# Optimization experiments

Hardware: AMD Instinct MI355X
Metric: run time of the kernel (lower is better)

## Reference

```python
import jax, jax.numpy as jnp
import numpy as np

F = 20000; S = 60000; U = 2000; I = 2000
NSUP = S + U + I
DEG = 8; E = NSUP * DEG
HID = 128; NH = 8; DH = HID // NH
SE = 256; UE = 128; IE = 128
FFN = 512; NITER = 1
SV = 100000; UV = 5000; IV = 5000


def _gat_ffn(h_src, h_dst, src, dst, ew, n_dst, W, al, ar, ae, W1, b1, W2, b2, g, b):
    # multi-head GAT with scalar edge-weight term + position-wise FFN (pre-LN residual)
    z_src = jnp.einsum('nd,hde->nhe', h_src, W)   # [Nsrc, NH, DH]
    z_dst = jnp.einsum('nd,hde->nhe', h_dst, W)   # [Ndst, NH, DH]
    el = jnp.einsum('nhe,he->nh', z_src, al)
    er = jnp.einsum('nhe,he->nh', z_dst, ar)
    e = jax.nn.leaky_relu(el[src] + er[dst] + ew[:, None] * ae[None, :], 0.2)  # [E, NH]
    m = jax.ops.segment_max(e, dst, num_segments=n_dst)
    m = jnp.where(jnp.isfinite(m), m, 0.0)
    ex = jnp.exp(e - m[dst])
    den = jax.ops.segment_sum(ex, dst, num_segments=n_dst)
    alpha = ex / jnp.maximum(den[dst], 1e-9)                       # edge softmax per dst
    out = jax.ops.segment_sum(alpha[:, :, None] * z_src[src], dst, num_segments=n_dst)
    h = jax.nn.elu(out.reshape(n_dst, NH * DH))
    mu = h.mean(-1, keepdims=True)
    v = ((h - mu) ** 2).mean(-1, keepdims=True)
    ln = (h - mu) * jax.lax.rsqrt(v + 1e-6) * g + b
    return h + (jnp.maximum(ln @ W1 + b1, 0.0) @ W2 + b2)


def setup_inputs() -> dict:
    key = jax.random.key(0)
    ks = jax.random.split(key, 40)
    d = {}
    d['fid'] = jax.random.randint(ks[0], (F,), 0, F)
    d['sid'] = jax.random.randint(ks[1], (S,), 0, SV)
    d['uid'] = jax.random.randint(ks[2], (U,), 0, UV)
    d['iid'] = jax.random.randint(ks[3], (I,), 0, IV)
    d['e_src'] = jax.random.randint(ks[4], (E,), 0, F)
    d['e_dst'] = jnp.repeat(jnp.arange(NSUP), DEG)   # fixed in-degree, every supernode covered
    d['e_w'] = jax.random.uniform(ks[5], (E,), jnp.float32)
    def n(i, shape, s=0.05):
        return jax.random.normal(ks[i], shape, jnp.float32) * s
    d['feat_tab'] = n(6, (F, HID), 1.0)
    d['sent_tab'] = n(7, (SV, SE), 1.0)
    d['user_tab'] = n(8, (UV, UE), 1.0)
    d['item_tab'] = n(9, (IV, IE), 1.0)
    d['Wsp'] = n(10, (SE, HID)); d['bsp'] = n(11, (HID,))
    d['Wup'] = n(12, (UE, HID)); d['Wip'] = n(13, (IE, HID))
    names = ['W', 'al', 'ar', 'ae', 'W1', 'b1', 'W2', 'b2', 'g', 'b']
    shapes = [(NH, HID, DH), (NH, DH), (NH, DH), (NH,), (HID, FFN), (FFN,), (FFN, HID), (HID,), (HID,), (HID,)]
    k = 14
    for pre in ['w2s_', 's2w_']:
        for nm, sh in zip(names, shapes):
            d[pre + nm] = n(k, sh); k += 1
    d['w2s_g'] = jnp.ones((HID,)); d['s2w_g'] = jnp.ones((HID,))
    d['whW'] = n(34, (HID, 2)); d['whb'] = n(35, (2,))
    return d


def reference(fid, sid, uid, iid, e_src, e_dst, e_w, feat_tab, sent_tab, user_tab, item_tab,
              Wsp, bsp, Wup, Wip,
              w2s_W, w2s_al, w2s_ar, w2s_ae, w2s_W1, w2s_b1, w2s_W2, w2s_b2, w2s_g, w2s_b,
              s2w_W, s2w_al, s2w_ar, s2w_ae, s2w_W1, s2w_b1, s2w_W2, s2w_b2, s2w_g, s2w_b,
              whW, whb):
    feat_init = feat_tab[fid]                     # feature init_state == its embedding
    sent_init = sent_tab[sid] @ Wsp + bsp         # sent_state_proj
    # mean of predecessor feature init_states per supernode (set_unembed / set_inembed)
    fsum = jax.ops.segment_sum(feat_init[e_src], e_dst, num_segments=NSUP)
    cnt = jax.ops.segment_sum(jnp.ones((E,), feat_init.dtype), e_dst, num_segments=NSUP)
    fmean = fsum / jnp.maximum(cnt, 1.0)[:, None]
    user_init = (user_tab[uid] + fmean[S:S + U]) @ Wup
    item_init = (item_tab[iid] + fmean[S + U:]) @ Wip
    sup = jnp.concatenate([sent_init, user_init, item_init], axis=0)  # [NSUP, HID]
    feat = feat_init
    p_w2s = (w2s_W, w2s_al, w2s_ar, w2s_ae, w2s_W1, w2s_b1, w2s_W2, w2s_b2, w2s_g, w2s_b)
    p_s2w = (s2w_W, s2w_al, s2w_ar, s2w_ae, s2w_W1, s2w_b1, s2w_W2, s2w_b2, s2w_g, s2w_b)
    sup = _gat_ffn(feat, sup, e_src, e_dst, e_w, NSUP, *p_w2s)        # feature2sent
    for _ in range(NITER):
        feat = _gat_ffn(sup, feat, e_dst, e_src, e_w, F, *p_s2w)      # sent2feature (reversed edges)
        sup = _gat_ffn(feat, sup, e_src, e_dst, e_w, NSUP, *p_w2s)    # feature2sent
    return sup[:S] @ whW + whb                    # wh on sentence nodes -> [S, 2]
```

## Files before the change

kernel.cpp:

```cpp
#include <hip/hip_runtime.h>
#include <hip/hip_bf16.h>

constexpr int F_N   = 20000;
constexpr int S_N   = 60000;
constexpr int U_N   = 2000;
constexpr int I_N   = 2000;
constexpr int NSUPN = 64000;
constexpr int E_NN  = NSUPN * 8;

typedef __bf16 bf16_t;
typedef bf16_t bf16x8 __attribute__((ext_vector_type(8)));
typedef float  f32x4  __attribute__((ext_vector_type(4)));


__global__ void k_gather128(const float* __restrict__ tab, const int* __restrict__ idx,
                            float* __restrict__ out, int M) {
  int t = blockIdx.x * 256 + threadIdx.x;
  if (t >= M * 128) return;
  int r = t >> 7, c = t & 127;
  out[t] = tab[(size_t)idx[r] * 128 + c];
}

__global__ void k_fmean(const float* __restrict__ feat, const int* __restrict__ esrc,
                        float* __restrict__ fm) {
  int n = S_N + blockIdx.x;
  int c = threadIdx.x;
  float s = 0.f;
#pragma unroll
  for (int j = 0; j < 8; ++j) s += feat[(size_t)esrc[n * 8 + j] * 128 + c];
  fm[(size_t)blockIdx.x * 128 + c] = s * 0.125f;
}

__global__ void k_addgather(const float* __restrict__ tab, const int* __restrict__ idx,
                            const float* __restrict__ fm, int fmoff,
                            float* __restrict__ out, int M) {
  int t = blockIdx.x * 256 + threadIdx.x;
  if (t >= M * 128) return;
  int r = t >> 7, c = t & 127;
  out[t] = tab[(size_t)idx[r] * 128 + c] + fm[(size_t)(fmoff + r) * 128 + c];
}

__global__ void k_conv_t_split(const float* __restrict__ in, bf16_t* __restrict__ hi,
                               bf16_t* __restrict__ lo, int K, int C) {
  int t = blockIdx.x * 256 + threadIdx.x;
  if (t >= K * C) return;
  int c = t / K, k = t - c * K;
  float v = in[(size_t)k * C + c];
  bf16_t h = (bf16_t)v;
  hi[t] = h;
  lo[t] = (bf16_t)(v - (float)h);
}

__global__ void k_build_wft_split(const float* __restrict__ W, bf16_t* __restrict__ hi,
                                  bf16_t* __restrict__ lo) {
  int t = blockIdx.x * 256 + threadIdx.x;
  if (t >= 128 * 128) return;
  int col = t >> 7, d = t & 127;
  float v = W[((col >> 4) << 11) + (d << 4) + (col & 15)];
  bf16_t h = (bf16_t)v;
  hi[t] = h;
  lo[t] = (bf16_t)(v - (float)h);
}

template<bool GATHER, bool BIAS>
__global__ __launch_bounds__(128)
void k_gemm_rows(const float* __restrict__ A, const int* __restrict__ gidx, int ldA,
                 const float* __restrict__ B, const float* __restrict__ bias,
                 float* __restrict__ C, int K) {
  __shared__ float As[16 * 256];
  int r0 = blockIdx.x * 16;
  int tid = threadIdx.x;
  for (int idx = tid; idx < 16 * K; idx += 128) {
    int r = idx / K, k = idx - r * K;
    int row = r0 + r;
    size_t abase = GATHER ? (size_t)gidx[row] * ldA : (size_t)row * ldA;
    As[r * K + k] = A[abase + k];
  }
  __syncthreads();
  float acc[16];
#pragma unroll
  for (int r = 0; r < 16; ++r) acc[r] = 0.f;
  int c = tid;
  for (int k = 0; k < K; ++k) {
    float w = B[k * 128 + c];
#pragma unroll
    for (int r = 0; r < 16; ++r) acc[r] += As[r * K + k] * w;
  }
  float bv = BIAS ? bias[c] : 0.f;
#pragma unroll
  for (int r = 0; r < 16; ++r) C[(size_t)(r0 + r) * 128 + c] = acc[r] + bv;
}

__global__ __launch_bounds__(256)
void k_sent_mfma(const float* __restrict__ tab, const int* __restrict__ sid,
                 const bf16_t* __restrict__ Bhi, const bf16_t* __restrict__ Blo,
                 const float* __restrict__ bias, float* __restrict__ out) {
  __shared__ bf16_t Ahi[32][256];
  __shared__ bf16_t Alo[32][256];
  int r0 = blockIdx.x * 32;
  int tid = threadIdx.x;
  for (int i = 0; i < 4; ++i) {
    int cid = tid + 256 * i;
    int r = cid >> 5, c0 = (cid & 31) * 8;
    const float* src = &tab[(size_t)sid[r0 + r] * 256 + c0];
    float4 v0 = *(const float4*)src, v1 = *(const float4*)(src + 4);
    float vv[8] = {v0.x, v0.y, v0.z, v0.w, v1.x, v1.y, v1.z, v1.w};
    bf16x8 hv, lv;
#pragma unroll
    for (int j = 0; j < 8; ++j) {
      bf16_t hb = (bf16_t)vv[j];
      hv[j] = hb;
      lv[j] = (bf16_t)(vv[j] - (float)hb);
    }
    int cs = c0 ^ ((r & 7) << 3);
    *(bf16x8*)&Ahi[r][cs] = hv;
    *(bf16x8*)&Alo[r][cs] = lv;
  }
  __syncthreads();
  int w = tid >> 6, l = tid & 63, la = l & 15, lb = l >> 4;
  int swz = (la & 7) << 3;
  f32x4 acc[2][2] = {};
#pragma unroll
  for (int ks = 0; ks < 8; ++ks) {
    int k0 = ks * 32 + lb * 8;
    int ka = k0 ^ swz;
    bf16x8 ah0 = *(const bf16x8*)&Ahi[la][ka];
    bf16x8 ah1 = *(const bf16x8*)&Ahi[16 + la][ka];
    bf16x8 al0 = *(const bf16x8*)&Alo[la][ka];
    bf16x8 al1 = *(const bf16x8*)&Alo[16 + la][ka];
#pragma unroll
    for (int ct = 0; ct < 2; ++ct) {
      int col = w * 32 + ct * 16 + la;
      bf16x8 bh = *(const bf16x8*)&Bhi[(size_t)col * 256 + k0];
      bf16x8 bl = *(const bf16x8*)&Blo[(size_t)col * 256 + k0];
      acc[0][ct] = __builtin_amdgcn_mfma_f32_16x16x32_bf16(ah0, bh, acc[0][ct], 0, 0, 0);
      acc[0][ct] = __builtin_amdgcn_mfma_f32_16x16x32_bf16(ah0, bl, acc[0][ct], 0, 0, 0);
      acc[0][ct] = __builtin_amdgcn_mfma_f32_16x16x32_bf16(al0, bh, acc[0][ct], 0, 0, 0);
      acc[1][ct] = __builtin_amdgcn_mfma_f32_16x16x32_bf16(ah1, bh, acc[1][ct], 0, 0, 0);
      acc[1][ct] = __builtin_amdgcn_mfma_f32_16x16x32_bf16(ah1, bl, acc[1][ct], 0, 0, 0);
      acc[1][ct] = __builtin_amdgcn_mfma_f32_16x16x32_bf16(al1, bh, acc[1][ct], 0, 0, 0);
    }
  }
#pragma unroll
  for (int ct = 0; ct < 2; ++ct) {
    int col = w * 32 + ct * 16 + la;
    float bv = bias[col];
#pragma unroll
    for (int rt = 0; rt < 2; ++rt)
#pragma unroll
      for (int r = 0; r < 4; ++r)
        out[(size_t)(r0 + rt * 16 + lb * 4 + r) * 128 + col] = acc[rt][ct][r] + bv;
  }
}

__global__ __launch_bounds__(256)
void k_zproj_mfma(const float* __restrict__ h, const bf16_t* __restrict__ WftH,
                  const bf16_t* __restrict__ WftL, float* __restrict__ z) {
  __shared__ bf16_t hbH[32][128];
  __shared__ bf16_t hbL[32][128];
  int r0 = blockIdx.x * 32;
  int tid = threadIdx.x;
  for (int i = 0; i < 2; ++i) {
    int cid = tid + 256 * i;
    int r = cid >> 4, c0 = (cid & 15) * 8;
    const float* src = &h[(size_t)(r0 + r) * 128 + c0];
    float4 v0 = *(const float4*)src;
    float4 v1 = *(const float4*)(src + 4);
    float vv[8] = {v0.x, v0.y, v0.z, v0.w, v1.x, v1.y, v1.z, v1.w};
    bf16x8 hv, lv;
#pragma unroll
    for (int j = 0; j < 8; ++j) {
      bf16_t hb = (bf16_t)vv[j];
      hv[j] = hb;
      lv[j] = (bf16_t)(vv[j] - (float)hb);
    }
    int cs = c0 ^ ((r & 7) << 3);
    *(bf16x8*)&hbH[r][cs] = hv;
    *(bf16x8*)&hbL[r][cs] = lv;
  }
  __syncthreads();
  int w = tid >> 6, l = tid & 63, la = l & 15, lb = l >> 4;
  int swz = (la & 7) << 3;
  f32x4 acc[2][2] = {};
#pragma unroll
  for (int ks = 0; ks < 4; ++ks) {
    int k0 = ks * 32 + lb * 8;
    int ka = k0 ^ swz;
    bf16x8 ah0 = *(const bf16x8*)&hbH[la][ka];
    bf16x8 ah1 = *(const bf16x8*)&hbH[16 + la][ka];
    bf16x8 al0 = *(const bf16x8*)&hbL[la][ka];
    bf16x8 al1 = *(const bf16x8*)&hbL[16 + la][ka];
#pragma unroll
    for (int ct = 0; ct < 2; ++ct) {
      int col = w * 32 + ct * 16 + la;
      bf16x8 bh = *(const bf16x8*)&WftH[(size_t)col * 128 + k0];
      bf16x8 bl = *(const bf16x8*)&WftL[(size_t)col * 128 + k0];
      acc[0][ct] = __builtin_amdgcn_mfma_f32_16x16x32_bf16(ah0, bh, acc[0][ct], 0, 0, 0);
      acc[0][ct] = __builtin_amdgcn_mfma_f32_16x16x32_bf16(ah0, bl, acc[0][ct], 0, 0, 0);
      acc[0][ct] = __builtin_amdgcn_mfma_f32_16x16x32_bf16(al0, bh, acc[0][ct], 0, 0, 0);
      acc[1][ct] = __builtin_amdgcn_mfma_f32_16x16x32_bf16(ah1, bh, acc[1][ct], 0, 0, 0);
      acc[1][ct] = __builtin_amdgcn_mfma_f32_16x16x32_bf16(ah1, bl, acc[1][ct], 0, 0, 0);
      acc[1][ct] = __builtin_amdgcn_mfma_f32_16x16x32_bf16(al1, bh, acc[1][ct], 0, 0, 0);
    }
  }
#pragma unroll
  for (int ct = 0; ct < 2; ++ct) {
    int col = w * 32 + ct * 16 + la;
#pragma unroll
    for (int rt = 0; rt < 2; ++rt)
#pragma unroll
      for (int r = 0; r < 4; ++r)
        z[(size_t)(r0 + rt * 16 + lb * 4 + r) * 128 + col] = acc[rt][ct][r];
  }
}

__global__ void k_el(const float* __restrict__ z, const float* __restrict__ a,
                     float* __restrict__ el, int N) {
  int t = blockIdx.x * 256 + threadIdx.x;
  if (t >= N * 8) return;
  int r = t >> 3, h = t & 7;
  const float* zr = z + (size_t)r * 128 + h * 16;
  const float* ah = a + h * 16;
  float s = 0.f;
#pragma unroll
  for (int e = 0; e < 16; ++e) s += zr[e] * ah[e];
  el[t] = s;
}

__global__ void k_logits_w2s(const float* __restrict__ el, const float* __restrict__ er,
                             const int* __restrict__ esrc, const float* __restrict__ ew,
                             const float* __restrict__ ae, float* __restrict__ lg) {
  int t = blockIdx.x * 256 + threadIdx.x;
  if (t >= E_NN * 8) return;
  int eid = t >> 3, h = t & 7;
  float x = el[(size_t)esrc[eid] * 8 + h] + er[(size_t)(eid >> 3) * 8 + h] + ew[eid] * ae[h];
  lg[t] = x > 0.f ? x : 0.2f * x;
}
__global__ void k_logits_s2w(const float* __restrict__ el, const float* __restrict__ er,
                             const int* __restrict__ eids, const int* __restrict__ pdst,
                             const float* __restrict__ ew, const float* __restrict__ ae,
                             float* __restrict__ lg) {
  int t = blockIdx.x * 256 + threadIdx.x;
  if (t >= E_NN * 8) return;
  int q = t >> 3, h = t & 7;
  int eid = eids[q];
  float x = el[(size_t)(eid >> 3) * 8 + h] + er[(size_t)pdst[q] * 8 + h] + ew[eid] * ae[h];
  lg[t] = x > 0.f ? x : 0.2f * x;
}

__global__ __launch_bounds__(256)
void k_attn8_v2(const float* __restrict__ zsrc, const float* __restrict__ lg,
                const int* __restrict__ esrc, float* __restrict__ hout) {
  int half = threadIdx.x >> 7;
  int n = blockIdx.x * 2 + half;
  int c = threadIdx.x & 127;
  int h = c >> 4;
  int s[8];
#pragma unroll
  for (int j = 0; j < 8; ++j) s[j] = esrc[n * 8 + j];
  float lv[8];
#pragma unroll
  for (int j = 0; j < 8; ++j) lv[j] = lg[(size_t)n * 64 + j * 8 + h];
  float m = -1e30f;
#pragma unroll
  for (int j = 0; j < 8; ++j) m = fmaxf(m, lv[j]);
  float den = 0.f;
#pragma unroll
  for (int j = 0; j < 8; ++j) { lv[j] = __expf(lv[j] - m); den += lv[j]; }
  float inv = 1.f / fmaxf(den, 1e-9f);
  float acc = 0.f;
#pragma unroll
  for (int j = 0; j < 8; ++j) acc += lv[j] * zsrc[(size_t)s[j] * 128 + c];
  acc *= inv;
  hout[(size_t)n * 128 + c] = acc > 0.f ? acc : (__expf(acc) - 1.f);
}

__global__ __launch_bounds__(128)
void k_attn_csr2(const float* __restrict__ zsrc, const float* __restrict__ lg,
                 const int* __restrict__ rowptr, const int* __restrict__ eids,
                 float* __restrict__ hout) {
  constexpr int CHUNK = 128;
  __shared__ float alg[CHUNK][8];
  __shared__ int   svs[CHUNK];
  int n = blockIdx.x;
  int c = threadIdx.x;
  int h = c >> 4;
  int beg = rowptr[n], deg = rowptr[n + 1] - beg;
  float acc = 0.f, mh = -1e30f, denh = 0.f;
  for (int c0 = 0; c0 < deg; c0 += CHUNK) {
    int cn = min(CHUNK, deg - c0);
    __syncthreads();
    for (int idx = c; idx < cn * 8; idx += 128)
      alg[idx >> 3][idx & 7] = lg[(size_t)(beg + c0) * 8 + idx];
    for (int j = c; j < cn; j += 128)
      svs[j] = eids[beg + c0 + j] >> 3;
    __syncthreads();
    float cm = mh;
    for (int j = 0; j < cn; ++j) cm = fmaxf(cm, alg[j][h]);
    float scale = __expf(mh - cm);
    acc *= scale; denh *= scale; mh = cm;
#pragma unroll 4
    for (int j = 0; j < cn; ++j) {
      float p = __expf(alg[j][h] - mh);
      denh += p;
      acc += p * zsrc[(size_t)svs[j] * 128 + c];
    }
  }
  acc /= fmaxf(denh, 1e-9f);
  hout[(size_t)n * 128 + c] = acc > 0.f ? acc : (__expf(acc) - 1.f);
}

__global__ __launch_bounds__(256)
void k_ln_ffn_mfma(const float* __restrict__ h, const float* __restrict__ g,
                   const float* __restrict__ b,
                   const bf16_t* __restrict__ W1tH, const bf16_t* __restrict__ W1tL,
                   const float* __restrict__ b1,
                   const bf16_t* __restrict__ W2tH, const bf16_t* __restrict__ W2tL,
                   const float* __restrict__ b2,
                   float* __restrict__ out) {
  __shared__ float  hs[32][128];
  __shared__ bf16_t lnbH[32][128];
  __shared__ bf16_t lnbL[32][128];
  __shared__ bf16_t mid[32][512];
  int r0 = blockIdx.x * 32;
  int tid = threadIdx.x;
  for (int i = 0; i < 4; ++i) {
    int cid = tid + 256 * i;
    int r = cid >> 5, c0 = (cid & 31) * 4;
    *(float4*)&hs[r][c0] = *(const float4*)&h[(size_t)(r0 + r) * 128 + c0];
  }
  __syncthreads();
  {
    int r = tid >> 3, lane = tid & 7;
    float sum = 0.f, sq = 0.f;
    for (int c = lane; c < 128; c += 8) { float v = hs[r][c]; sum += v; sq += v * v; }
#pragma unroll
    for (int o = 4; o >= 1; o >>= 1) { sum += __shfl_xor(sum, o); sq += __shfl_xor(sq, o); }
    float mu = sum * (1.f / 128.f);
    float var = sq * (1.f / 128.f) - mu * mu;
    float inv = rsqrtf(var + 1e-6f);
    int sw = (r & 7) << 3;
    for (int c = lane; c < 128; c += 8) {
      float v = (hs[r][c] - mu) * inv * g[c] + b[c];
      bf16_t hh = (bf16_t)v;
      lnbH[r][c ^ sw] = hh;
      lnbL[r][c ^ sw] = (bf16_t)(v - (float)hh);
    }
  }
  __syncthreads();
  int w = tid >> 6, l = tid & 63, la = l & 15, lb = l >> 4;
  int swz = (la & 7) << 3;
  {
    f32x4 acc1[2][8] = {};
#pragma unroll
    for (int ks = 0; ks < 4; ++ks) {
      int k0 = ks * 32 + lb * 8;
      int ka = k0 ^ swz;
      bf16x8 ah0 = *(const bf16x8*)&lnbH[la][ka];
      bf16x8 ah1 = *(const bf16x8*)&lnbH[16 + la][ka];
      bf16x8 al0 = *(const bf16x8*)&lnbL[la][ka];
      bf16x8 al1 = *(const bf16x8*)&lnbL[16 + la][ka];
#pragma unroll
      for (int ct = 0; ct < 8; ++ct) {
        int col = w * 128 + ct * 16 + la;
        bf16x8 bh = *(const bf16x8*)&W1tH[(size_t)col * 128 + k0];
        bf16x8 bl = *(const bf16x8*)&W1tL[(size_t)col * 128 + k0];
        acc1[0][ct] = __builtin_amdgcn_mfma_f32_16x16x32_bf16(ah0, bh, acc1[0][ct], 0, 0, 0);
        acc1[0][ct] = __builtin_amdgcn_mfma_f32_16x16x32_bf16(ah0, bl, acc1[0][ct], 0, 0, 0);
        acc1[0][ct] = __builtin_amdgcn_mfma_f32_16x16x32_bf16(al0, bh, acc1[0][ct], 0, 0, 0);
        acc1[1][ct] = __builtin_amdgcn_mfma_f32_16x16x32_bf16(ah1, bh, acc1[1][ct], 0, 0, 0);
        acc1[1][ct] = __builtin_amdgcn_mfma_f32_16x16x32_bf16(ah1, bl, acc1[1][ct], 0, 0, 0);
        acc1[1][ct] = __builtin_amdgcn_mfma_f32_16x16x32_bf16(al1, bh, acc1[1][ct], 0, 0, 0);
      }
    }
#pragma unroll
    for (int ct = 0; ct < 8; ++ct) {
      int col = w * 128 + ct * 16 + la;
      float bv = b1[col];
#pragma unroll
      for (int rt = 0; rt < 2; ++rt)
#pragma unroll
        for (int r = 0; r < 4; ++r) {
          int row = rt * 16 + lb * 4 + r;
          float v = acc1[rt][ct][r] + bv;
          mid[row][col ^ ((row & 7) << 3)] = (bf16_t)fmaxf(v, 0.f);
        }
    }
  }
  __syncthreads();
  {
    f32x4 acc2[2][2] = {};
#pragma unroll
    for (int ks = 0; ks < 16; ++ks) {
      int k0 = ks * 32 + lb * 8;
      int ka = k0 ^ swz;
      bf16x8 a0 = *(const bf16x8*)&mid[la][ka];
      bf16x8 a1 = *(const bf16x8*)&mid[16 + la][ka];
#pragma unroll
      for (int ct = 0; ct < 2; ++ct) {
        int col = w * 32 + ct * 16 + la;
        bf16x8 bh = *(const bf16x8*)&W2tH[(size_t)col * 512 + k0];
        bf16x8 bl = *(const bf16x8*)&W2tL[(size_t)col * 512 + k0];
        acc2[0][ct] = __builtin_amdgcn_mfma_f32_16x16x32_bf16(a0, bh, acc2[0][ct], 0, 0, 0);
        acc2[0][ct] = __builtin_amdgcn_mfma_f32_16x16x32_bf16(a0, bl, acc2[0][ct], 0, 0, 0);
        acc2[1][ct] = __builtin_amdgcn_mfma_f32_16x16x32_bf16(a1, bh, acc2[1][ct], 0, 0, 0);
        acc2[1][ct] = __builtin_amdgcn_mfma_f32_16x16x32_bf16(a1, bl, acc2[1][ct], 0, 0, 0);
      }
    }
#pragma unroll
    for (int ct = 0; ct < 2; ++ct) {
      int col = w * 32 + ct * 16 + la;
      float bv = b2[col];
#pragma unroll
      for (int rt = 0; rt < 2; ++rt)
#pragma unroll
        for (int r = 0; r < 4; ++r) {
          int row = rt * 16 + lb * 4 + r;
          out[(size_t)(r0 + row) * 128 + col] = hs[row][col] + acc2[rt][ct][r] + bv;
        }
    }
  }
}

__global__ __launch_bounds__(256)
void k_whout(const float* __restrict__ sup, const float* __restrict__ whW,
             const float* __restrict__ whb, float* __restrict__ out) {
  int wv = threadIdx.x >> 6, lane = threadIdx.x & 63;
  int r = blockIdx.x * 4 + wv;
  if (r >= S_N) return;
  const float* row = sup + (size_t)r * 128;
  float a0 = 0.f, a1 = 0.f;
  for (int d = lane; d < 128; d += 64) {
    float v = row[d];
    a0 += v * whW[d * 2];
    a1 += v * whW[d * 2 + 1];
  }
#pragma unroll
  for (int o = 32; o >= 1; o >>= 1) { a0 += __shfl_xor(a0, o); a1 += __shfl_xor(a1, o); }
  if (lane == 0) { out[r * 2] = a0 + whb[0]; out[r * 2 + 1] = a1 + whb[1]; }
}

__global__ void k_count(const int* __restrict__ esrc, int* __restrict__ counts) {
  int t = blockIdx.x * 256 + threadIdx.x;
  if (t < E_NN) atomicAdd(&counts[esrc[t]], 1);
}

__global__ __launch_bounds__(1024)
void k_scan(const int* __restrict__ counts, int* __restrict__ rowptr) {
  __shared__ int wsum[16];
  __shared__ int carry;
  int tid = threadIdx.x, lane = tid & 63, w = tid >> 6;
  if (tid == 0) { carry = 0; rowptr[0] = 0; }
  __syncthreads();
  for (int base = 0; base < F_N; base += 1024) {
    int i = base + tid;
    int v = (i < F_N) ? counts[i] : 0;
    int s = v;
#pragma unroll
    for (int o = 1; o < 64; o <<= 1) { int t2 = __shfl_up(s, o); if (lane >= o) s += t2; }
    if (lane == 63) wsum[w] = s;
    __syncthreads();
    if (w == 0) {
      int t2 = (lane < 16) ? wsum[lane] : 0;
#pragma unroll
      for (int o = 1; o < 16; o <<= 1) { int u = __shfl_up(t2, o); if (lane >= o) t2 += u; }
      if (lane < 16) wsum[lane] = t2;
    }
    __syncthreads();
    int add = carry + (w > 0 ? wsum[w - 1] : 0);
    if (i < F_N) rowptr[i + 1] = s + add;
    int total = wsum[15];
    __syncthreads();
    if (tid == 0) carry += total;
    __syncthreads();
  }
}

__global__ void k_fill(const int* __restrict__ esrc, const int* __restrict__ rowptr,
                       int* __restrict__ fill, int* __restrict__ eids,
                       int* __restrict__ pdst) {
  int t = blockIdx.x * 256 + threadIdx.x;
  if (t < E_NN) {
    int sv = esrc[t];
    int p = atomicAdd(&fill[sv], 1);
    eids[rowptr[sv] + p] = t;
    pdst[rowptr[sv] + p] = sv;
  }
}

extern "C" void kernel_launch(void* const* d_in, const int* in_sizes, int n_in,
                              void* d_out, int out_size, void* d_ws, size_t ws_size,
                              hipStream_t stream) {
  const int* fid = (const int*)d_in[0];
  const int* sid = (const int*)d_in[1];
  const int* uid = (const int*)d_in[2];
  const int* iid = (const int*)d_in[3];
  const int* e_src = (const int*)d_in[4];
  const int* e_dst = (const int*)d_in[5];
  const float* e_w = (const float*)d_in[6];
  const float* feat_tab = (const float*)d_in[7];
  const float* sent_tab = (const float*)d_in[8];
  const float* user_tab = (const float*)d_in[9];
  const float* item_tab = (const float*)d_in[10];
  const float* Wsp = (const float*)d_in[11];
  const float* bsp = (const float*)d_in[12];
  const float* Wup = (const float*)d_in[13];
  const float* Wip = (const float*)d_in[14];
  const float* w2s[10]; for (int i = 0; i < 10; ++i) w2s[i] = (const float*)d_in[15 + i];
  const float* s2w[10]; for (int i = 0; i < 10; ++i) s2w[i] = (const float*)d_in[25 + i];
  const float* whW = (const float*)d_in[35];
  const float* whb = (const float*)d_in[36];
  float* out = (float*)d_out;

  char* wp = (char*)d_ws;
  auto alloc = [&](size_t nbytes) -> void* {
    void* p = (void*)wp;
    wp += (nbytes + 255) & ~(size_t)255;
    return p;
  };
  bf16_t* WftHA = (bf16_t*)alloc(128 * 128 * 2);
  bf16_t* WftLA = (bf16_t*)alloc(128 * 128 * 2);
  bf16_t* WftHB = (bf16_t*)alloc(128 * 128 * 2);
  bf16_t* WftLB = (bf16_t*)alloc(128 * 128 * 2);
  bf16_t* W1tHA = (bf16_t*)alloc(512 * 128 * 2);
  bf16_t* W1tLA = (bf16_t*)alloc(512 * 128 * 2);
  bf16_t* W1tHB = (bf16_t*)alloc(512 * 128 * 2);
  bf16_t* W1tLB = (bf16_t*)alloc(512 * 128 * 2);
  bf16_t* W2tHA = (bf16_t*)alloc(512 * 128 * 2);
  bf16_t* W2tLA = (bf16_t*)alloc(512 * 128 * 2);
  bf16_t* W2tHB = (bf16_t*)alloc(512 * 128 * 2);
  bf16_t* W2tLB = (bf16_t*)alloc(512 * 128 * 2);
  bf16_t* WspH  = (bf16_t*)alloc(128 * 256 * 2);
  bf16_t* WspL  = (bf16_t*)alloc(128 * 256 * 2);
  int* rowptr  = (int*)alloc((size_t)(F_N + 1) * 4);
  int* cnts    = (int*)alloc((size_t)2 * F_N * 4);
  int* eids    = (int*)alloc((size_t)E_NN * 4);
  int* pdst    = (int*)alloc((size_t)E_NN * 4);
  float* featA = (float*)alloc((size_t)F_N * 128 * 4);
  float* supA  = (float*)alloc((size_t)NSUPN * 128 * 4);
  float* zf    = (float*)alloc((size_t)F_N * 128 * 4);
  float* zs    = (float*)alloc((size_t)NSUPN * 128 * 4);
  float* hbuf  = (float*)alloc((size_t)NSUPN * 128 * 4);
  float* elbig = (float*)alloc((size_t)NSUPN * 8 * 4);
  float* erbig = (float*)alloc((size_t)NSUPN * 8 * 4);
  float* lgbuf = (float*)alloc((size_t)E_NN * 8 * 4);
  float* atmpu = (float*)alloc((size_t)U_N * 128 * 4);
  float* atmpi = (float*)alloc((size_t)I_N * 128 * 4);
  float* fm    = (float*)alloc((size_t)(U_N + I_N) * 128 * 4);

  k_build_wft_split<<<64, 256, 0, stream>>>(w2s[0], WftHA, WftLA);
  k_build_wft_split<<<64, 256, 0, stream>>>(s2w[0], WftHB, WftLB);
  k_conv_t_split<<<(512 * 128 + 255) / 256, 256, 0, stream>>>(w2s[4], W1tHA, W1tLA, 128, 512);
  k_conv_t_split<<<(512 * 128 + 255) / 256, 256, 0, stream>>>(s2w[4], W1tHB, W1tLB, 128, 512);
  k_conv_t_split<<<(512 * 128 + 255) / 256, 256, 0, stream>>>(w2s[6], W2tHA, W2tLA, 512, 128);
  k_conv_t_split<<<(512 * 128 + 255) / 256, 256, 0, stream>>>(s2w[6], W2tHB, W2tLB, 512, 128);
  k_conv_t_split<<<(256 * 128 + 255) / 256, 256, 0, stream>>>(Wsp, WspH, WspL, 256, 128);

  k_gather128<<<(F_N * 128 + 255) / 256, 256, 0, stream>>>(feat_tab, fid, featA, F_N);
  k_fmean<<<U_N + I_N, 128, 0, stream>>>(featA, e_src, fm);
  k_sent_mfma<<<S_N / 32, 256, 0, stream>>>(sent_tab, sid, WspH, WspL, bsp, supA);
  k_addgather<<<(U_N * 128 + 255) / 256, 256, 0, stream>>>(user_tab, uid, fm, 0, atmpu, U_N);
  k_gemm_rows<false, false><<<U_N / 16, 128, 0, stream>>>(atmpu, nullptr, 128, Wup, nullptr,
                                                          supA + (size_t)S_N * 128, 128);
  k_addgather<<<(I_N * 128 + 255) / 256, 256, 0, stream>>>(item_tab, iid, fm, U_N, atmpi, I_N);
  k_gemm_rows<false, false><<<I_N / 16, 128, 0, stream>>>(atmpi, nullptr, 128, Wip, nullptr,
                                                          supA + (size_t)(S_N + U_N) * 128, 128);
  hipMemsetAsync(cnts, 0, (size_t)2 * F_N * 4, stream);
  k_count<<<(E_NN + 255) / 256, 256, 0, stream>>>(e_src, cnts);
  k_scan<<<1, 1024, 0, stream>>>(cnts, rowptr);
  k_fill<<<(E_NN + 255) / 256, 256, 0, stream>>>(e_src, rowptr, cnts + F_N, eids, pdst);

  auto gat_w2s = [&](const float* hsrc, const float* hdst, float* outp) {
    k_zproj_mfma<<<F_N / 32, 256, 0, stream>>>(hsrc, WftHA, WftLA, zf);
    k_zproj_mfma<<<NSUPN / 32, 256, 0, stream>>>(hdst, WftHA, WftLA, zs);
    k_el<<<(F_N * 8 + 255) / 256, 256, 0, stream>>>(zf, w2s[1], elbig, F_N);
    k_el<<<(NSUPN * 8 + 255) / 256, 256, 0, stream>>>(zs, w2s[2], erbig, NSUPN);
    k_logits_w2s<<<(E_NN * 8 + 255) / 256, 256, 0, stream>>>(elbig, erbig, e_src, e_w, w2s[3], lgbuf);
    k_attn8_v2<<<NSUPN / 2, 256, 0, stream>>>(zf, lgbuf, e_src, hbuf);
    k_ln_ffn_mfma<<<NSUPN / 32, 256, 0, stream>>>(hbuf, w2s[8], w2s[9], W1tHA, W1tLA, w2s[5],
                                                  W2tHA, W2tLA, w2s[7], outp);
  };
  auto gat_s2w = [&](const float* hsrc, const float* hdst, float* outp) {
    k_zproj_mfma<<<NSUPN / 32, 256, 0, stream>>>(hsrc, WftHB, WftLB, zs);
    k_zproj_mfma<<<F_N / 32, 256, 0, stream>>>(hdst, WftHB, WftLB, zf);
    k_el<<<(NSUPN * 8 + 255) / 256, 256, 0, stream>>>(zs, s2w[1], elbig, NSUPN);
    k_el<<<(F_N * 8 + 255) / 256, 256, 0, stream>>>(zf, s2w[2], erbig, F_N);
    k_logits_s2w<<<(E_NN * 8 + 255) / 256, 256, 0, stream>>>(elbig, erbig, eids, pdst, e_w, s2w[3], lgbuf);
    k_attn_csr2<<<F_N, 128, 0, stream>>>(zs, lgbuf, rowptr, eids, hbuf);
    k_ln_ffn_mfma<<<F_N / 32, 256, 0, stream>>>(hbuf, s2w[8], s2w[9], W1tHB, W1tLB, s2w[5],
                                                W2tHB, W2tLB, s2w[7], outp);
  };

  gat_w2s(featA, supA, supA);
  gat_s2w(supA, featA, featA);
  gat_w2s(featA, supA, supA);

  k_whout<<<(S_N + 3) / 4, 256, 0, stream>>>(supA, whW, whb, out);
}
```

Before: 783.4 us.

## Skip non-sentence rows in final GAT, rework LN-FFN tile, sort CSR rows

New measurement: 1.064 ms. +35.9%, slower.

```diff
diff --git a/kernel.cpp b/kernel.cpp
--- a/kernel.cpp
+++ b/kernel.cpp
@@ -1,5 +1,6 @@
 #include <hip/hip_runtime.h>
 #include <hip/hip_bf16.h>
+#include <math.h>
 
 constexpr int F_N   = 20000;
 constexpr int S_N   = 60000;
@@ -229,9 +230,9 @@
 
 __global__ void k_logits_w2s(const float* __restrict__ el, const float* __restrict__ er,
                              const int* __restrict__ esrc, const float* __restrict__ ew,
-                             const float* __restrict__ ae, float* __restrict__ lg) {
-  int t = blockIdx.x * 256 + threadIdx.x;
-  if (t >= E_NN * 8) return;
+                             const float* __restrict__ ae, float* __restrict__ lg, int nE) {
+  int t = blockIdx.x * 256 + threadIdx.x;
+  if (t >= nE * 8) return;
   int eid = t >> 3, h = t & 7;
   float x = el[(size_t)esrc[eid] * 8 + h] + er[(size_t)(eid >> 3) * 8 + h] + ew[eid] * ae[h];
   lg[t] = x > 0.f ? x : 0.2f * x;
@@ -266,13 +267,13 @@
   for (int j = 0; j < 8; ++j) m = fmaxf(m, lv[j]);
   float den = 0.f;
 #pragma unroll
-  for (int j = 0; j < 8; ++j) { lv[j] = __expf(lv[j] - m); den += lv[j]; }
+  for (int j = 0; j < 8; ++j) { lv[j] = expf(lv[j] - m); den += lv[j]; }
   float inv = 1.f / fmaxf(den, 1e-9f);
   float acc = 0.f;
 #pragma unroll
   for (int j = 0; j < 8; ++j) acc += lv[j] * zsrc[(size_t)s[j] * 128 + c];
   acc *= inv;
-  hout[(size_t)n * 128 + c] = acc > 0.f ? acc : (__expf(acc) - 1.f);
+  hout[(size_t)n * 128 + c] = acc > 0.f ? acc : expm1f(acc);
 }
 
 __global__ __launch_bounds__(128)
@@ -297,80 +298,88 @@
     __syncthreads();
     float cm = mh;
     for (int j = 0; j < cn; ++j) cm = fmaxf(cm, alg[j][h]);
-    float scale = __expf(mh - cm);
+    float scale = expf(mh - cm);
     acc *= scale; denh *= scale; mh = cm;
 #pragma unroll 4
     for (int j = 0; j < cn; ++j) {
-      float p = __expf(alg[j][h] - mh);
+      float p = expf(alg[j][h] - mh);
       denh += p;
       acc += p * zsrc[(size_t)svs[j] * 128 + c];
     }
   }
   acc /= fmaxf(denh, 1e-9f);
-  hout[(size_t)n * 128 + c] = acc > 0.f ? acc : (__expf(acc) - 1.f);
-}
-
-__global__ __launch_bounds__(256)
-void k_ln_ffn_mfma(const float* __restrict__ h, const float* __restrict__ g,
-                   const float* __restrict__ b,
-                   const bf16_t* __restrict__ W1tH, const bf16_t* __restrict__ W1tL,
-                   const float* __restrict__ b1,
-                   const bf16_t* __restrict__ W2tH, const bf16_t* __restrict__ W2tL,
-                   const float* __restrict__ b2,
-                   float* __restrict__ out) {
-  __shared__ float  hs[32][128];
-  __shared__ bf16_t lnbH[32][128];
-  __shared__ bf16_t lnbL[32][128];
-  __shared__ bf16_t mid[32][512];
-  int r0 = blockIdx.x * 32;
+  hout[(size_t)n * 128 + c] = acc > 0.f ? acc : expm1f(acc);
+}
+
+__global__ __launch_bounds__(256, 4)
+void k_ln_ffn3(const float* __restrict__ h, const float* __restrict__ g,
+               const float* __restrict__ b,
+               const bf16_t* __restrict__ W1tH, const bf16_t* __restrict__ W1tL,
+               const float* __restrict__ b1,
+               const bf16_t* __restrict__ W2tH, const bf16_t* __restrict__ W2tL,
+               const float* __restrict__ b2,
+               float* __restrict__ out) {
+  __shared__ bf16_t lnbH[16][128];
+  __shared__ bf16_t lnbL[16][128];
+  __shared__ bf16_t midH[16][512];
+  __shared__ bf16_t midL[16][512];
+  int r0 = blockIdx.x * 16;
   int tid = threadIdx.x;
-  for (int i = 0; i < 4; ++i) {
-    int cid = tid + 256 * i;
-    int r = cid >> 5, c0 = (cid & 31) * 4;
-    *(float4*)&hs[r][c0] = *(const float4*)&h[(size_t)(r0 + r) * 128 + c0];
-  }
-  __syncthreads();
   {
-    int r = tid >> 3, lane = tid & 7;
-    float sum = 0.f, sq = 0.f;
-    for (int c = lane; c < 128; c += 8) { float v = hs[r][c]; sum += v; sq += v * v; }
-#pragma unroll
-    for (int o = 4; o >= 1; o >>= 1) { sum += __shfl_xor(sum, o); sq += __shfl_xor(sq, o); }
+    int r = tid >> 4, lane = tid & 15;
+    int c0 = lane * 8;
+    const float* hrow = &h[(size_t)(r0 + r) * 128 + c0];
+    float4 t0 = *(const float4*)hrow;
+    float4 t1 = *(const float4*)(hrow + 4);
+    float v[8] = {t0.x, t0.y, t0.z, t0.w, t1.x, t1.y, t1.z, t1.w};
+    float sum = 0.f;
+#pragma unroll
+    for (int j = 0; j < 8; ++j) sum += v[j];
+#pragma unroll
+    for (int o = 8; o >= 1; o >>= 1) sum += __shfl_xor(sum, o);
     float mu = sum * (1.f / 128.f);
-    float var = sq * (1.f / 128.f) - mu * mu;
-    float inv = rsqrtf(var + 1e-6f);
-    int sw = (r & 7) << 3;
-    for (int c = lane; c < 128; c += 8) {
-      float v = (hs[r][c] - mu) * inv * g[c] + b[c];
-      bf16_t hh = (bf16_t)v;
-      lnbH[r][c ^ sw] = hh;
-      lnbL[r][c ^ sw] = (bf16_t)(v - (float)hh);
-    }
+    float sq = 0.f;
+#pragma unroll
+    for (int j = 0; j < 8; ++j) { float d = v[j] - mu; sq += d * d; }
+#pragma unroll
+    for (int o = 8; o >= 1; o >>= 1) sq += __shfl_xor(sq, o);
+    float var = sq * (1.f / 128.f);
+    float inv = 1.f / sqrtf(var + 1e-6f);
+    float4 gv0 = *(const float4*)(g + c0), gv1 = *(const float4*)(g + c0 + 4);
+    float4 bv0 = *(const float4*)(b + c0), bv1 = *(const float4*)(b + c0 + 4);
+    float gg[8] = {gv0.x, gv0.y, gv0.z, gv0.w, gv1.x, gv1.y, gv1.z, gv1.w};
+    float bb[8] = {bv0.x, bv0.y, bv0.z, bv0.w, bv1.x, bv1.y, bv1.z, bv1.w};
+    bf16x8 ho, lo;
+#pragma unroll
+    for (int j = 0; j < 8; ++j) {
+      float lnv = (v[j] - mu) * inv * gg[j] + bb[j];
+      bf16_t hh = (bf16_t)lnv;
+      ho[j] = hh;
+      lo[j] = (bf16_t)(lnv - (float)hh);
+    }
+    int cs = c0 ^ ((r & 7) << 3);
+    *(bf16x8*)&lnbH[r][cs] = ho;
+    *(bf16x8*)&lnbL[r][cs] = lo;
   }
   __syncthreads();
   int w = tid >> 6, l = tid & 63, la = l & 15, lb = l >> 4;
   int swz = (la & 7) << 3;
   {
-    f32x4 acc1[2][8] = {};
+    f32x4 acc1[8] = {};
 #pragma unroll
     for (int ks = 0; ks < 4; ++ks) {
       int k0 = ks * 32 + lb * 8;
       int ka = k0 ^ swz;
-      bf16x8 ah0 = *(const bf16x8*)&lnbH[la][ka];
-      bf16x8 ah1 = *(const bf16x8*)&lnbH[16 + la][ka];
-      bf16x8 al0 = *(const bf16x8*)&lnbL[la][ka];
-      bf16x8 al1 = *(const bf16x8*)&lnbL[16 + la][ka];
+      bf16x8 ah = *(const bf16x8*)&lnbH[la][ka];
+      bf16x8 al = *(const bf16x8*)&lnbL[la][ka];
 #pragma unroll
       for (int ct = 0; ct < 8; ++ct) {
         int col = w * 128 + ct * 16 + la;
         bf16x8 bh = *(const bf16x8*)&W1tH[(size_t)col * 128 + k0];
         bf16x8 bl = *(const bf16x8*)&W1tL[(size_t)col * 128 + k0];
-        acc1[0][ct] = __builtin_amdgcn_mfma_f32_16x16x32_bf16(ah0, bh, acc1[0][ct], 0, 0, 0);
-        acc1[0][ct] = __builtin_amdgcn_mfma_f32_16x16x32_bf16(ah0, bl, acc1[0][ct], 0, 0, 0);
-        acc1[0][ct] = __builtin_amdgcn_mfma_f32_16x16x32_bf16(al0, bh, acc1[0][ct], 0, 0, 0);
-        acc1[1][ct] = __builtin_amdgcn_mfma_f32_16x16x32_bf16(ah1, bh, acc1[1][ct], 0, 0, 0);
-        acc1[1][ct] = __builtin_amdgcn_mfma_f32_16x16x32_bf16(ah1, bl, acc1[1][ct], 0, 0, 0);
-        acc1[1][ct] = __builtin_amdgcn_mfma_f32_16x16x32_bf16(al1, bh, acc1[1][ct], 0, 0, 0);
+        acc1[ct] = __builtin_amdgcn_mfma_f32_16x16x32_bf16(ah, bh, acc1[ct], 0, 0, 0);
+        acc1[ct] = __builtin_amdgcn_mfma_f32_16x16x32_bf16(ah, bl, acc1[ct], 0, 0, 0);
+        acc1[ct] = __builtin_amdgcn_mfma_f32_16x16x32_bf16(al, bh, acc1[ct], 0, 0, 0);
       }
     }
 #pragma unroll
@@ -378,46 +387,43 @@
       int col = w * 128 + ct * 16 + la;
       float bv = b1[col];
 #pragma unroll
-      for (int rt = 0; rt < 2; ++rt)
-#pragma unroll
-        for (int r = 0; r < 4; ++r) {
-          int row = rt * 16 + lb * 4 + r;
-          float v = acc1[rt][ct][r] + bv;
-          mid[row][col ^ ((row & 7) << 3)] = (bf16_t)fmaxf(v, 0.f);
-        }
+      for (int r = 0; r < 4; ++r) {
+        int row = lb * 4 + r;
+        float v = fmaxf(acc1[ct][r] + bv, 0.f);
+        bf16_t hh = (bf16_t)v;
+        int cs = col ^ ((row & 7) << 3);
+        midH[row][cs] = hh;
+        midL[row][cs] = (bf16_t)(v - (float)hh);
+      }
     }
   }
   __syncthreads();
-  {
-    f32x4 acc2[2][2] = {};
-#pragma unroll
-    for (int ks = 0; ks < 16; ++ks) {
-      int k0 = ks * 32 + lb * 8;
-      int ka = k0 ^ swz;
-      bf16x8 a0 = *(const bf16x8*)&mid[la][ka];
-      bf16x8 a1 = *(const bf16x8*)&mid[16 + la][ka];
-#pragma unroll
-      for (int ct = 0; ct < 2; ++ct) {
-        int col = w * 32 + ct * 16 + la;
-        bf16x8 bh = *(const bf16x8*)&W2tH[(size_t)col * 512 + k0];
-        bf16x8 bl = *(const bf16x8*)&W2tL[(size_t)col * 512 + k0];
-        acc2[0][ct] = __builtin_amdgcn_mfma_f32_16x16x32_bf16(a0, bh, acc2[0][ct], 0, 0, 0);
-        acc2[0][ct] = __builtin_amdgcn_mfma_f32_16x16x32_bf16(a0, bl, acc2[0][ct], 0, 0, 0);
-        acc2[1][ct] = __builtin_amdgcn_mfma_f32_16x16x32_bf16(a1, bh, acc2[1][ct], 0, 0, 0);
-        acc2[1][ct] = __builtin_amdgcn_mfma_f32_16x16x32_bf16(a1, bl, acc2[1][ct], 0, 0, 0);
-      }
-    }
+  f32x4 acc2[2] = {};
+#pragma unroll
+  for (int ks = 0; ks < 16; ++ks) {
+    int k0 = ks * 32 + lb * 8;
+    int ka = k0 ^ swz;
+    bf16x8 ah = *(const bf16x8*)&midH[la][ka];
+    bf16x8 al = *(const bf16x8*)&midL[la][ka];
 #pragma unroll
     for (int ct = 0; ct < 2; ++ct) {
       int col = w * 32 + ct * 16 + la;
-      float bv = b2[col];
-#pragma unroll
-      for (int rt = 0; rt < 2; ++rt)
-#pragma unroll
-        for (int r = 0; r < 4; ++r) {
-          int row = rt * 16 + lb * 4 + r;
-          out[(size_t)(r0 + row) * 128 + col] = hs[row][col] + acc2[rt][ct][r] + bv;
-        }
+      bf16x8 bh = *(const bf16x8*)&W2tH[(size_t)col * 512 + k0];
+      bf16x8 bl = *(const bf16x8*)&W2tL[(size_t)col * 512 + k0];
+      acc2[ct] = __builtin_amdgcn_mfma_f32_16x16x32_bf16(ah, bh, acc2[ct], 0, 0, 0);
+      acc2[ct] = __builtin_amdgcn_mfma_f32_16x16x32_bf16(ah, bl, acc2[ct], 0, 0, 0);
+      acc2[ct] = __builtin_amdgcn_mfma_f32_16x16x32_bf16(al, bh, acc2[ct], 0, 0, 0);
+    }
+  }
+#pragma unroll
+  for (int ct = 0; ct < 2; ++ct) {
+    int col = w * 32 + ct * 16 + la;
+    float bv = b2[col];
+#pragma unroll
+    for (int r = 0; r < 4; ++r) {
+      int row = lb * 4 + r;
+      size_t gi = (size_t)(r0 + row) * 128 + col;
+      out[gi] = h[gi] + acc2[ct][r] + bv;
     }
   }
 }
@@ -486,6 +492,32 @@
     eids[rowptr[sv] + p] = t;
     pdst[rowptr[sv] + p] = sv;
   }
+}
+
+__global__ __launch_bounds__(256)
+void k_sort_rows(const int* __restrict__ rowptr, int* __restrict__ eids) {
+  __shared__ int buf[1024];
+  int n = blockIdx.x;
+  int beg = rowptr[n], deg = rowptr[n + 1] - beg;
+  if (deg <= 1 || deg > 1024) return;
+  int m = 1; while (m < deg) m <<= 1;
+  for (int i = threadIdx.x; i < m; i += 256)
+    buf[i] = (i < deg) ? eids[beg + i] : 0x7fffffff;
+  __syncthreads();
+  for (int k = 2; k <= m; k <<= 1) {
+    for (int j = k >> 1; j > 0; j >>= 1) {
+      for (int i = threadIdx.x; i < m; i += 256) {
+        int ixj = i ^ j;
+        if (ixj > i) {
+          int a = buf[i], bv = buf[ixj];
+          bool up = ((i & k) == 0);
+          if ((a > bv) == up) { buf[i] = bv; buf[ixj] = a; }
+        }
+      }
+      __syncthreads();
+    }
+  }
+  for (int i = threadIdx.x; i < deg; i += 256) eids[beg + i] = buf[i];
 }
 
 extern "C" void kernel_launch(void* const* d_in, const int* in_sizes, int n_in,
@@ -569,16 +601,19 @@
   k_count<<<(E_NN + 255) / 256, 256, 0, stream>>>(e_src, cnts);
   k_scan<<<1, 1024, 0, stream>>>(cnts, rowptr);
   k_fill<<<(E_NN + 255) / 256, 256, 0, stream>>>(e_src, rowptr, cnts + F_N, eids, pdst);
-
-  auto gat_w2s = [&](const float* hsrc, const float* hdst, float* outp) {
+  k_sort_rows<<<F_N, 256, 0, stream>>>(rowptr, eids);
+
+  auto gat_w2s = [&](const float* hsrc, const float* hdst, float* outp, bool last) {
+    int ndst = last ? S_N : NSUPN;
     k_zproj_mfma<<<F_N / 32, 256, 0, stream>>>(hsrc, WftHA, WftLA, zf);
-    k_zproj_mfma<<<NSUPN / 32, 256, 0, stream>>>(hdst, WftHA, WftLA, zs);
+    k_zproj_mfma<<<ndst / 32, 256, 0, stream>>>(hdst, WftHA, WftLA, zs);
     k_el<<<(F_N * 8 + 255) / 256, 256, 0, stream>>>(zf, w2s[1], elbig, F_N);
-    k_el<<<(NSUPN * 8 + 255) / 256, 256, 0, stream>>>(zs, w2s[2], erbig, NSUPN);
-    k_logits_w2s<<<(E_NN * 8 + 255) / 256, 256, 0, stream>>>(elbig, erbig, e_src, e_w, w2s[3], lgbuf);
-    k_attn8_v2<<<NSUPN / 2, 256, 0, stream>>>(zf, lgbuf, e_src, hbuf);
-    k_ln_ffn_mfma<<<NSUPN / 32, 256, 0, stream>>>(hbuf, w2s[8], w2s[9], W1tHA, W1tLA, w2s[5],
-                                                  W2tHA, W2tLA, w2s[7], outp);
+    k_el<<<(ndst * 8 + 255) / 256, 256, 0, stream>>>(zs, w2s[2], erbig, ndst);
+    k_logits_w2s<<<(ndst * 8 * 8 + 255) / 256, 256, 0, stream>>>(elbig, erbig, e_src, e_w,
+                                                                 w2s[3], lgbuf, ndst * 8);
+    k_attn8_v2<<<ndst / 2, 256, 0, stream>>>(zf, lgbuf, e_src, hbuf);
+    k_ln_ffn3<<<ndst / 16, 256, 0, stream>>>(hbuf, w2s[8], w2s[9], W1tHA, W1tLA, w2s[5],
+                                             W2tHA, W2tLA, w2s[7], outp);
   };
   auto gat_s2w = [&](const float* hsrc, const float* hdst, float* outp) {
     k_zproj_mfma<<<NSUPN / 32, 256, 0, stream>>>(hsrc, WftHB, WftLB, zs);
@@ -587,13 +622,13 @@
     k_el<<<(F_N * 8 + 255) / 256, 256, 0, stream>>>(zf, s2w[2], erbig, F_N);
     k_logits_s2w<<<(E_NN * 8 + 255) / 256, 256, 0, stream>>>(elbig, erbig, eids, pdst, e_w, s2w[3], lgbuf);
     k_attn_csr2<<<F_N, 128, 0, stream>>>(zs, lgbuf, rowptr, eids, hbuf);
-    k_ln_ffn_mfma<<<F_N / 32, 256, 0, stream>>>(hbuf, s2w[8], s2w[9], W1tHB, W1tLB, s2w[5],
-                                                W2tHB, W2tLB, s2w[7], outp);
+    k_ln_ffn3<<<F_N / 16, 256, 0, stream>>>(hbuf, s2w[8], s2w[9], W1tHB, W1tLB, s2w[5],
+                                            W2tHB, W2tLB, s2w[7], outp);
   };
 
-  gat_w2s(featA, supA, supA);
+  gat_w2s(featA, supA, supA, false);
   gat_s2w(supA, featA, featA);
-  gat_w2s(featA, supA, supA);
+  gat_w2s(featA, supA, supA, true);
 
   k_whout<<<(S_N + 3) / 4, 256, 0, stream>>>(supA, whW, whb, out);
 }
```
